# Optimization experiments

Measured on AMD Instinct MI355X. Metric: run time of the kernel, lower is better.

## Reference

```python
import jax, jax.numpy as jnp
import numpy as np

SR_CUT = 10.0
N_ATOMS = 10000
N_PAIRS = 250000
K = 128          # radial basis size
H = 128          # interaction / output hidden width
NB = 5           # num_blocks
NIL = 2          # num_interaction_layers
NOL = 2          # num_output_layers
NO = 2           # num_outputs


def setup_inputs() -> dict:
    key = jax.random.key(0)
    ks = jax.random.split(key, 10)
    Z = jax.random.randint(ks[0], (N_ATOMS,), 0, 95)
    R = jax.random.normal(ks[1], (N_ATOMS, 3), dtype=jnp.float32) * 3.0
    idx_i = jnp.sort(jax.random.randint(ks[2], (N_PAIRS,), 0, N_ATOMS))
    idx_j = jax.random.randint(ks[3], (N_PAIRS,), 0, N_ATOMS)
    s = 0.05
    iW = jax.random.normal(ks[4], (NB, NIL, H, H), dtype=jnp.float32) * s
    iB = jnp.zeros((NB, NIL, H), dtype=jnp.float32)
    oW = jax.random.normal(ks[5], (NB, NOL, H, H), dtype=jnp.float32) * s
    oB = jnp.zeros((NB, NOL, H), dtype=jnp.float32)
    oWf = jax.random.normal(ks[6], (NB, H, NO), dtype=jnp.float32) * s
    oBf = jnp.zeros((NB, NO), dtype=jnp.float32)
    scales = jnp.ones((NO, 95), dtype=jnp.float32)
    shifts = jnp.zeros((NO, 95), dtype=jnp.float32)
    return {"Z": Z, "R": R, "idx_i": idx_i, "idx_j": idx_j,
            "iW": iW, "iB": iB, "oW": oW, "oB": oB,
            "oWf": oWf, "oBf": oBf, "scales": scales, "shifts": shifts}


def _ssp(x):
    # shifted softplus: softplus(x) - log(2)
    return jax.nn.softplus(x) - jnp.log(2.0).astype(x.dtype)


def _basis(rij):
    # smooth polynomial cutoff + Gaussian basis on exp(-r) (PhysNet-style 'Default' radial basis)
    x = rij / SR_CUT
    fcut = jnp.where(rij < SR_CUT, 1.0 - 6.0 * x**5 + 15.0 * x**4 - 10.0 * x**3, 0.0)
    mu = jnp.linspace(np.exp(-SR_CUT), 1.0, K, dtype=rij.dtype)          # [K]
    width = ((2.0 / K) * (1.0 - np.exp(-SR_CUT))) ** (-2)
    er = jnp.exp(-rij)[:, None]                                          # [P,1]
    return fcut[:, None] * jnp.exp(-width * (er - mu) ** 2)              # [P,K]


def reference(Z, R, idx_i, idx_j, iW, iB, oW, oB, oWf, oBf, scales, shifts):
    # pairwise distances via gather (bf_layer.getPairs)
    D = R[idx_j] - R[idx_i]                                              # [P,3]
    rij = jnp.sqrt(jnp.sum(D * D, axis=-1) + 1e-12)                      # [P]
    bf = _basis(rij)                                                     # [P,K]

    x = bf
    outputs = jnp.zeros((N_ATOMS, NO), dtype=R.dtype)
    nhloss = jnp.zeros((), dtype=R.dtype)
    lastout2 = None
    for b in range(NB):
        # interaction block: per-edge MLP (K==H so stacked weights are uniform)
        for l in range(NIL):
            x = _ssp(x @ iW[b, l] + iB[b, l])
        # output block: per-edge MLP + final linear head
        y = x
        for l in range(NOL):
            y = _ssp(y @ oW[b, l] + oB[b, l])
        out_e = y @ oWf[b] + oBf[b]                                      # [P,NO]
        out = jax.ops.segment_sum(out_e, idx_i, num_segments=N_ATOMS)    # [N,NO]
        outputs = outputs + out
        out2 = out ** 2
        if b > 0:
            nhloss = nhloss + jnp.mean(out2 / (out2 + lastout2 + 1e-7))
        lastout2 = out2

    sc = scales[:, Z].T                                                  # [N,NO]
    sh = shifts[:, Z].T                                                  # [N,NO]
    outputs = outputs * sc + sh
    return outputs, rij, nhloss
```

## Files before the change

kernel.cpp:

```cpp
#include <hip/hip_runtime.h>
#include <stdint.h>

#define NP   250000
#define NA   10000
#define NBLK 5
#define NL   20
#define BLOB_W_BYTES 16384
#define BLOB_BYTES   16896

#define LOG2E 1.4426950408889634f
#define LN2   0.6931471805599453f

typedef float  f32x4  __attribute__((ext_vector_type(4)));
typedef unsigned short ushort_t;
typedef unsigned int   uint_t;
typedef int4  i4_ma __attribute__((may_alias));
typedef uint2 u2_ma __attribute__((may_alias));
typedef uint_t u1_ma __attribute__((may_alias));

#if __has_builtin(__builtin_amdgcn_exp2f)
#define FEXP2(x) __builtin_amdgcn_exp2f(x)
#else
#define FEXP2(x) exp2f(x)
#endif
#if __has_builtin(__builtin_amdgcn_logf)
#define FLOG2(x) __builtin_amdgcn_logf(x)
#else
#define FLOG2(x) log2f(x)
#endif

__device__ uint8_t g_blob[NL * BLOB_BYTES];
__device__ float   g_outs[NBLK * NA * 2];
__device__ float   g_nh[1];
__device__ float   g_Rf[NA * 3];
__device__ float   g_oWfF[NBLK * 128 * 2];
__device__ float   g_oBfF[NBLK * 2];
__device__ float   g_scF[190];
__device__ float   g_shF[190];

static __device__ __forceinline__ float bf2f(ushort_t u) {
    return __uint_as_float(((uint_t)u) << 16);
}
static __device__ uint8_t f2fp8(float f) {
    uint_t u = __float_as_uint(f);
    uint8_t s = (uint8_t)((u >> 24) & 0x80);
    float af = fabsf(f);
    if (af != af) return (uint8_t)(s | 0x7F);
    if (af > 448.0f) return (uint8_t)(s | 0x7E);
    int e = (int)((u >> 23) & 0xFF) - 127;
    uint_t m = u & 0x7FFFFFu;
    if (e >= -6) {
        uint_t mant = m >> 20;
        uint_t rest = m & 0xFFFFFu;
        if (rest > 0x80000u || (rest == 0x80000u && (mant & 1u))) mant++;
        uint_t ee = (uint_t)(e + 7);
        if (mant == 8u) { mant = 0u; ee++; }
        if (ee > 15u || (ee == 15u && mant > 6u)) return (uint8_t)(s | 0x7E);
        return (uint8_t)(s | (ee << 3) | mant);
    }
    int qq = (int)rintf(af * 512.0f);
    if (qq > 7) return (uint8_t)(s | 0x08);
    return (uint8_t)(s | (uint_t)qq);
}
template <bool HI>
static __device__ __forceinline__ int cvtpk2(float a, float b, int old) {
#if __has_builtin(__builtin_amdgcn_cvt_pk_fp8_f32)
    return __builtin_amdgcn_cvt_pk_fp8_f32(a, b, old, HI);
#else
    int p = (int)f2fp8(a) | ((int)f2fp8(b) << 8);
    return HI ? (int)((old & 0x0000FFFF) | ((uint_t)p << 16))
              : (int)((old & 0xFFFF0000) | (uint_t)p);
#endif
}
static __device__ __forceinline__ long u2l(u2_ma v) {
    union { u2_ma u; long l; } x; x.u = v; return x.l;
}
static __device__ __forceinline__ float ssp_u(float accv) {
    return FLOG2(0.5f + FEXP2(accv));
}

static __device__ __forceinline__ bool detect_is_f32(const ushort_t* probe) {
    __shared__ int flag;
    if (threadIdx.x == 0) flag = 0;
    __syncthreads();
    if (threadIdx.x < 256) {
        float v = fabsf(bf2f(probe[2 * threadIdx.x]));
        if (!(v <= 64.0f)) flag = 1;
    }
    __syncthreads();
    return flag != 0;
}
static __device__ __forceinline__ float in_elt(const void* p, int i, bool isf32) {
    return isf32 ? ((const float*)p)[i] : bf2f(((const ushort_t*)p)[i]);
}

__global__ void prep_weights(const void* __restrict__ iW, const void* __restrict__ iB,
                             const void* __restrict__ oW, const void* __restrict__ oB)
{
    const bool isf32 = detect_is_f32((const ushort_t*)iW);
    const int L = blockIdx.x >> 2;
    const int qr = blockIdx.x & 3;
    const int b = L >> 2, li = L & 3;
    const void* srcW = (li < 2) ? iW : oW;
    const void* srcB = (li < 2) ? iB : oB;
    const int lyr = (li < 2) ? (b * 2 + li) : (b * 2 + li - 2);
    const int wofs = lyr * 16384;
    const int bofs = lyr * 128;
    uint8_t* blob = g_blob + (size_t)L * BLOB_BYTES;
    uint8_t* dw = blob;
    float*   db = (float*)(blob + BLOB_W_BYTES);
    for (int t = threadIdx.x; t < 4096; t += blockDim.x) {
        int idx = qr * 4096 + t;
        int k = idx >> 7, n = idx & 127;
        float w = in_elt(srcW, wofs + k * 128 + n, isf32);
        if (L == 0) w *= LOG2E;
        dw[n * 128 + 8 * ((k >> 3) ^ (n & 15)) + (k & 7)] = f2fp8(w);
    }
    if (qr == 0)
        for (int m = threadIdx.x; m < 128; m += blockDim.x)
            db[m] = in_elt(srcB, bofs + m, isf32) * LOG2E - 1.0f;
}

__global__ void prep_misc(const void* __restrict__ R, const void* __restrict__ oWf,
                          const void* __restrict__ oBf, const void* __restrict__ scales,
                          const void* __restrict__ shifts, const void* __restrict__ iW)
{
    const bool isf32 = detect_is_f32((const ushort_t*)iW);
    const int t = blockIdx.x * 256 + threadIdx.x;
    if (t < NBLK * NA * 2) g_outs[t] = 0.0f;
    if (t == 0)          g_nh[0]  = 0.0f;
    if (t < NA * 3)      g_Rf[t]   = in_elt(R, t, isf32);
    if (t < NBLK * 256)  g_oWfF[t] = LN2 * in_elt(oWf, t, isf32);
    if (t < NBLK * 2)    g_oBfF[t] = in_elt(oBf, t, isf32);
    if (t < 190)         g_scF[t]  = in_elt(scales, t, isf32);
    if (t < 190)         g_shF[t]  = in_elt(shifts, t, isf32);
}

__global__ __launch_bounds__(256, 3)
void pairs_mlp_kernel(const int* __restrict__ idx_i,
                      const int* __restrict__ idx_j,
                      float* __restrict__ out_rij)
{
    __shared__ i4_ma w_lds[1024];
    __shared__ u2_ma act_all[4 * 512];

    const int wave = threadIdx.x >> 6;
    const int lane = threadIdx.x & 63;
    u2_ma* act = act_all + wave * 512;
    const u2_ma* wl2 = (const u2_ma*)w_lds;

    const int pp = lane & 31;
    const int p0 = blockIdx.x * 128 + wave * 32;
    const int p = p0 + pp;
    const bool valid = (p < NP);

    int ai = 0, aj = 0;
    if (valid) { ai = idx_i[p]; aj = idx_j[p]; }
    float xi0 = g_Rf[3 * ai + 0], xi1 = g_Rf[3 * ai + 1], xi2 = g_Rf[3 * ai + 2];
    float xj0 = g_Rf[3 * aj + 0], xj1 = g_Rf[3 * aj + 1], xj2 = g_Rf[3 * aj + 2];
    float dx = xj0 - xi0, dy = xj1 - xi1, dz = xj2 - xi2;
    float rij = sqrtf(dx * dx + dy * dy + dz * dz + 1e-12f);
    if (lane < 32 && valid) out_rij[p] = rij;

    float fcut = 0.0f;
    if (valid && rij < 10.0f) {
        float xc = rij * 0.1f;
        float x3 = xc * xc * xc;
        fcut = 1.0f + x3 * (-10.0f + xc * (15.0f - 6.0f * xc));
    }
    const float mu0 = 4.5399929762484854e-05f;
    const float dmu = (1.0f - mu0) / 127.0f;
    const float wc = (2.0f / 128.0f) * (1.0f - mu0);
    const float NW2 = -(1.0f / (wc * wc)) * LOG2E;
    float er = FEXP2(-rij * LOG2E);

    const int q = lane >> 4;
    const int l15 = lane & 15;
    const int aseg = valid ? ai : -1;

    u2_ma bfrX[2][4];
    {
        float er_n[2], fc_n[2];
        er_n[0] = __shfl(er, l15, 64);      fc_n[0] = __shfl(fcut, l15, 64);
        er_n[1] = __shfl(er, 16 + l15, 64); fc_n[1] = __shfl(fcut, 16 + l15, 64);
#pragma unroll
        for (int nt = 0; nt < 2; ++nt)
#pragma unroll
            for (int kt = 0; kt < 4; ++kt) {
                float v[8];
#pragma unroll
                for (int jj = 0; jj < 8; ++jj) {
                    int g = kt * 32 + q * 8 + jj;
                    float mu = mu0 + (float)g * dmu;
                    float e0 = er_n[nt] - mu;
                    v[jj] = fc_n[nt] * FEXP2(NW2 * e0 * e0);
                }
                int w0 = cvtpk2<false>(v[0], v[1], 0);
                w0 = cvtpk2<true>(v[2], v[3], w0);
                int w1 = cvtpk2<false>(v[4], v[5], 0);
                w1 = cvtpk2<true>(v[6], v[7], w1);
                bfrX[nt][kt].x = (uint_t)w0;
                bfrX[nt][kt].y = (uint_t)w1;
            }
    }

    for (int blk = 0; blk < NBLK; ++blk) {
#pragma unroll
        for (int li = 0; li < 4; ++li) {
            const int L = blk * 4 + li;
            const i4_ma* gW = (const i4_ma*)(g_blob + (size_t)L * BLOB_BYTES);
            const float* bb = (const float*)(g_blob + (size_t)L * BLOB_BYTES + BLOB_W_BYTES);

            __syncthreads();
#pragma unroll
            for (int it = 0; it < 4; ++it)
                w_lds[threadIdx.x + it * 256] = gW[threadIdx.x + it * 256];
            __syncthreads();

            f32x4 acc[2][8];
#pragma unroll
            for (int mt = 0; mt < 8; ++mt) {
                const f32x4 bias = *(const f32x4*)(bb + mt * 16 + q * 4);
                acc[0][mt] = bias;
                acc[1][mt] = bias;
            }
#pragma unroll
            for (int kt = 0; kt < 4; ++kt) {
                const int cc = kt * 4 + q;
                u2_ma b0, b1;
                if (li == 0) {
                    b0 = bfrX[0][kt];
                    b1 = bfrX[1][kt];
                } else {
                    b0 = act[(l15) * 16 + (cc ^ l15)];
                    b1 = act[(16 + l15) * 16 + (cc ^ l15)];
                    if (li == 2) { bfrX[0][kt] = b0; bfrX[1][kt] = b1; }
                }
                const long lb0 = u2l(b0), lb1 = u2l(b1);
#pragma unroll
                for (int mt = 0; mt < 8; ++mt) {
                    const long la = u2l(wl2[(mt * 16 + l15) * 16 + (cc ^ l15)]);
                    acc[0][mt] = __builtin_amdgcn_mfma_f32_16x16x32_fp8_fp8(
                        la, lb0, acc[0][mt], 0, 0, 0);
                    acc[1][mt] = __builtin_amdgcn_mfma_f32_16x16x32_fp8_fp8(
                        la, lb1, acc[1][mt], 0, 0, 0);
                }
            }

            if (li < 3) {
#pragma unroll
                for (int mt = 0; mt < 8; ++mt) {
                    const int c = mt * 2 + (q >> 1);
#pragma unroll
                    for (int nt = 0; nt < 2; ++nt) {
                        float u0 = ssp_u(acc[nt][mt][0]);
                        float u1 = ssp_u(acc[nt][mt][1]);
                        float u2 = ssp_u(acc[nt][mt][2]);
                        float u3 = ssp_u(acc[nt][mt][3]);
                        int w = cvtpk2<false>(u0, u1, 0);
                        w = cvtpk2<true>(u2, u3, w);
                        const int rp = nt * 16 + l15;
                        ((u1_ma*)&act[rp * 16 + (c ^ (rp & 15))])[q & 1] = (uint_t)w;
                    }
                }
            } else {
                const float* hw = g_oWfF + blk * 256;
                const float ob0 = g_oBfF[blk * 2 + 0];
                const float ob1 = g_oBfF[blk * 2 + 1];
                float hs[2][2];
#pragma unroll
                for (int nt = 0; nt < 2; ++nt) {
                    float h0 = 0.f, h1 = 0.f;
#pragma unroll
                    for (int mt = 0; mt < 8; ++mt) {
#pragma unroll
                        for (int rr = 0; rr < 4; ++rr) {
                            float u = ssp_u(acc[nt][mt][rr]);
                            const int f = mt * 16 + q * 4 + rr;
                            h0 = fmaf(u, hw[f * 2 + 0], h0);
                            h1 = fmaf(u, hw[f * 2 + 1], h1);
                        }
                    }
                    h0 += __shfl_xor(h0, 16, 64);
                    h0 += __shfl_xor(h0, 32, 64);
                    h1 += __shfl_xor(h1, 16, 64);
                    h1 += __shfl_xor(h1, 32, 64);
                    hs[nt][0] = h0; hs[nt][1] = h1;
                }
                float c0v = (pp < 16) ? hs[0][0] : hs[1][0];
                float c1v = (pp < 16) ? hs[0][1] : hs[1][1];
                c0v += ob0; c1v += ob1;
#pragma unroll
                for (int d = 1; d < 32; d <<= 1) {
                    float t0 = __shfl_up(c0v, d, 64);
                    float t1 = __shfl_up(c1v, d, 64);
                    int   an = __shfl_up(aseg, d, 64);
                    if (pp >= d && an == aseg) { c0v += t0; c1v += t1; }
                }
                int ain = __shfl_down(aseg, 1, 64);
                bool tail = (pp == 31) || (ain != aseg);
                if (lane < 32 && valid && tail) {
                    atomicAdd(&g_outs[(blk * NA + aseg) * 2 + 0], c0v);
                    atomicAdd(&g_outs[(blk * NA + aseg) * 2 + 1], c1v);
                }
            }
        }
    }
}

__global__ void finalize_kernel(const int* __restrict__ Z,
                                float* __restrict__ out_atoms)
{
    __shared__ float red[256];
    const int a = blockIdx.x * 256 + threadIdx.x;
    float s = 0.f;
    if (a < NA) {
        float v[NBLK][2];
        float t0 = 0.f, t1 = 0.f;
#pragma unroll
        for (int b = 0; b < NBLK; ++b) {
            v[b][0] = g_outs[(b * NA + a) * 2 + 0];
            v[b][1] = g_outs[(b * NA + a) * 2 + 1];
            t0 += v[b][0]; t1 += v[b][1];
        }
        const int z = Z[a];
        out_atoms[a * 2 + 0] = t0 * g_scF[z]      + g_shF[z];
        out_atoms[a * 2 + 1] = t1 * g_scF[95 + z] + g_shF[95 + z];
#pragma unroll
        for (int b = 1; b < NBLK; ++b)
#pragma unroll
            for (int o = 0; o < 2; ++o) {
                float x2 = v[b][o] * v[b][o];
                float p2 = v[b - 1][o] * v[b - 1][o];
                s += x2 / (x2 + p2 + 1e-7f);
            }
    }
    red[threadIdx.x] = s;
    __syncthreads();
    for (int st = 128; st > 0; st >>= 1) {
        if (threadIdx.x < st) red[threadIdx.x] += red[threadIdx.x + st];
        __syncthreads();
    }
    if (threadIdx.x == 0) atomicAdd(&g_nh[0], red[0]);
}

__global__ void nh_write(float* __restrict__ out_nh)
{
    out_nh[0] = g_nh[0] * (1.0f / 20000.0f);
}

extern "C" void kernel_launch(void* const* d_in, const int* in_sizes, int n_in,
                              void* d_out, int out_size, void* d_ws, size_t ws_size,
                              hipStream_t stream)
{
    const int* Z     = (const int*)d_in[0];
    const void* R    = d_in[1];
    const int* idx_i = (const int*)d_in[2];
    const int* idx_j = (const int*)d_in[3];
    const void* iW   = d_in[4];
    const void* iB   = d_in[5];
    const void* oW   = d_in[6];
    const void* oB   = d_in[7];
    const void* oWf  = d_in[8];
    const void* oBf  = d_in[9];
    const void* scales = d_in[10];
    const void* shifts = d_in[11];

    float* out_f = (float*)d_out;

    prep_weights<<<NL * 4, 256, 0, stream>>>(iW, iB, oW, oB);
    prep_misc<<<(NBLK * NA * 2 + 255) / 256, 256, 0, stream>>>(R, oWf, oBf, scales, shifts, iW);
    pairs_mlp_kernel<<<(NP + 127) / 128, 256, 0, stream>>>(idx_i, idx_j, out_f + 2 * NA);
    finalize_kernel<<<(NA + 255) / 256, 256, 0, stream>>>(Z, out_f);
    nh_write<<<1, 1, 0, stream>>>(out_f + 2 * NA + NP);
}
```

Before: 279.6 us.

## Halve per-wave pair tile to 16 pairs and raise occupancy to four blocks

Each wave now handles 16 pairs instead of 32. Accumulators, activation LDS and basis registers are halved, and launch bounds are raised to allow 4 blocks per CU. The weight prep kernel now packs four fp8 weights per 32-bit store instead of writing single bytes, and the bias is fed directly as the first MFMA accumulator. The trade-off is that each weight tile staged in LDS is reused across half as many pairs, so weight loads and barriers per pair double, in exchange for lower register pressure and more waves resident.

```diff
diff --git a/kernel.cpp b/kernel.cpp
--- a/kernel.cpp
+++ b/kernel.cpp
@@ -107,14 +107,19 @@
     const int wofs = lyr * 16384;
     const int bofs = lyr * 128;
     uint8_t* blob = g_blob + (size_t)L * BLOB_BYTES;
-    uint8_t* dw = blob;
-    float*   db = (float*)(blob + BLOB_W_BYTES);
-    for (int t = threadIdx.x; t < 4096; t += blockDim.x) {
-        int idx = qr * 4096 + t;
-        int k = idx >> 7, n = idx & 127;
-        float w = in_elt(srcW, wofs + k * 128 + n, isf32);
-        if (L == 0) w *= LOG2E;
-        dw[n * 128 + 8 * ((k >> 3) ^ (n & 15)) + (k & 7)] = f2fp8(w);
+    uint_t* dw = (uint_t*)blob;
+    float*  db = (float*)(blob + BLOB_W_BYTES);
+    const float sc = (L == 0) ? LOG2E : 1.0f;
+    for (int t = threadIdx.x; t < 1024; t += blockDim.x) {
+        int d = qr * 1024 + t;
+        int n = d & 127, kg = d >> 7;
+        float w0 = sc * in_elt(srcW, wofs + (kg * 4 + 0) * 128 + n, isf32);
+        float w1 = sc * in_elt(srcW, wofs + (kg * 4 + 1) * 128 + n, isf32);
+        float w2 = sc * in_elt(srcW, wofs + (kg * 4 + 2) * 128 + n, isf32);
+        float w3 = sc * in_elt(srcW, wofs + (kg * 4 + 3) * 128 + n, isf32);
+        int w = cvtpk2<false>(w0, w1, 0);
+        w = cvtpk2<true>(w2, w3, w);
+        dw[n * 32 + 2 * ((kg >> 1) ^ (n & 15)) + (kg & 1)] = (uint_t)w;
     }
     if (qr == 0)
         for (int m = threadIdx.x; m < 128; m += blockDim.x)
@@ -136,22 +141,23 @@
     if (t < 190)         g_shF[t]  = in_elt(shifts, t, isf32);
 }
 
-__global__ __launch_bounds__(256, 3)
+__global__ __launch_bounds__(256, 4)
 void pairs_mlp_kernel(const int* __restrict__ idx_i,
                       const int* __restrict__ idx_j,
                       float* __restrict__ out_rij)
 {
     __shared__ i4_ma w_lds[1024];
-    __shared__ u2_ma act_all[4 * 512];
+    __shared__ u2_ma act_all[4 * 256];
 
     const int wave = threadIdx.x >> 6;
     const int lane = threadIdx.x & 63;
-    u2_ma* act = act_all + wave * 512;
+    u2_ma* act = act_all + wave * 256;
     const u2_ma* wl2 = (const u2_ma*)w_lds;
 
-    const int pp = lane & 31;
-    const int p0 = blockIdx.x * 128 + wave * 32;
-    const int p = p0 + pp;
+    const int q = lane >> 4;
+    const int l15 = lane & 15;
+    const int p0 = blockIdx.x * 64 + wave * 16;
+    const int p = p0 + l15;
     const bool valid = (p < NP);
 
     int ai = 0, aj = 0;
@@ -160,7 +166,7 @@
     float xj0 = g_Rf[3 * aj + 0], xj1 = g_Rf[3 * aj + 1], xj2 = g_Rf[3 * aj + 2];
     float dx = xj0 - xi0, dy = xj1 - xi1, dz = xj2 - xi2;
     float rij = sqrtf(dx * dx + dy * dy + dz * dz + 1e-12f);
-    if (lane < 32 && valid) out_rij[p] = rij;
+    if (lane < 16 && valid) out_rij[p] = rij;
 
     float fcut = 0.0f;
     if (valid && rij < 10.0f) {
@@ -174,34 +180,25 @@
     const float NW2 = -(1.0f / (wc * wc)) * LOG2E;
     float er = FEXP2(-rij * LOG2E);
 
-    const int q = lane >> 4;
-    const int l15 = lane & 15;
     const int aseg = valid ? ai : -1;
 
-    u2_ma bfrX[2][4];
-    {
-        float er_n[2], fc_n[2];
-        er_n[0] = __shfl(er, l15, 64);      fc_n[0] = __shfl(fcut, l15, 64);
-        er_n[1] = __shfl(er, 16 + l15, 64); fc_n[1] = __shfl(fcut, 16 + l15, 64);
-#pragma unroll
-        for (int nt = 0; nt < 2; ++nt)
-#pragma unroll
-            for (int kt = 0; kt < 4; ++kt) {
-                float v[8];
-#pragma unroll
-                for (int jj = 0; jj < 8; ++jj) {
-                    int g = kt * 32 + q * 8 + jj;
-                    float mu = mu0 + (float)g * dmu;
-                    float e0 = er_n[nt] - mu;
-                    v[jj] = fc_n[nt] * FEXP2(NW2 * e0 * e0);
-                }
-                int w0 = cvtpk2<false>(v[0], v[1], 0);
-                w0 = cvtpk2<true>(v[2], v[3], w0);
-                int w1 = cvtpk2<false>(v[4], v[5], 0);
-                w1 = cvtpk2<true>(v[6], v[7], w1);
-                bfrX[nt][kt].x = (uint_t)w0;
-                bfrX[nt][kt].y = (uint_t)w1;
-            }
+    u2_ma bfrX[4];
+#pragma unroll
+    for (int kt = 0; kt < 4; ++kt) {
+        float v[8];
+#pragma unroll
+        for (int jj = 0; jj < 8; ++jj) {
+            int g = kt * 32 + q * 8 + jj;
+            float mu = mu0 + (float)g * dmu;
+            float e0 = er - mu;
+            v[jj] = fcut * FEXP2(NW2 * e0 * e0);
+        }
+        int w0 = cvtpk2<false>(v[0], v[1], 0);
+        w0 = cvtpk2<true>(v[2], v[3], w0);
+        int w1 = cvtpk2<false>(v[4], v[5], 0);
+        w1 = cvtpk2<true>(v[6], v[7], w1);
+        bfrX[kt].x = (uint_t)w0;
+        bfrX[kt].y = (uint_t)w1;
     }
 
     for (int blk = 0; blk < NBLK; ++blk) {
@@ -217,33 +214,28 @@
                 w_lds[threadIdx.x + it * 256] = gW[threadIdx.x + it * 256];
             __syncthreads();
 
-            f32x4 acc[2][8];
-#pragma unroll
-            for (int mt = 0; mt < 8; ++mt) {
-                const f32x4 bias = *(const f32x4*)(bb + mt * 16 + q * 4);
-                acc[0][mt] = bias;
-                acc[1][mt] = bias;
-            }
+            f32x4 bias[8];
+#pragma unroll
+            for (int mt = 0; mt < 8; ++mt)
+                bias[mt] = *(const f32x4*)(bb + mt * 16 + q * 4);
+
+            f32x4 acc[8];
 #pragma unroll
             for (int kt = 0; kt < 4; ++kt) {
                 const int cc = kt * 4 + q;
-                u2_ma b0, b1;
+                u2_ma b0;
                 if (li == 0) {
-                    b0 = bfrX[0][kt];
-                    b1 = bfrX[1][kt];
+                    b0 = bfrX[kt];
                 } else {
-                    b0 = act[(l15) * 16 + (cc ^ l15)];
-                    b1 = act[(16 + l15) * 16 + (cc ^ l15)];
-                    if (li == 2) { bfrX[0][kt] = b0; bfrX[1][kt] = b1; }
-                }
-                const long lb0 = u2l(b0), lb1 = u2l(b1);
+                    b0 = act[l15 * 16 + (cc ^ l15)];
+                    if (li == 2) bfrX[kt] = b0;
+                }
+                const long lb0 = u2l(b0);
 #pragma unroll
                 for (int mt = 0; mt < 8; ++mt) {
                     const long la = u2l(wl2[(mt * 16 + l15) * 16 + (cc ^ l15)]);
-                    acc[0][mt] = __builtin_amdgcn_mfma_f32_16x16x32_fp8_fp8(
-                        la, lb0, acc[0][mt], 0, 0, 0);
-                    acc[1][mt] = __builtin_amdgcn_mfma_f32_16x16x32_fp8_fp8(
-                        la, lb1, acc[1][mt], 0, 0, 0);
+                    acc[mt] = __builtin_amdgcn_mfma_f32_16x16x32_fp8_fp8(
+                        la, lb0, (kt == 0) ? bias[mt] : acc[mt], 0, 0, 0);
                 }
             }
 
@@ -251,55 +243,45 @@
 #pragma unroll
                 for (int mt = 0; mt < 8; ++mt) {
                     const int c = mt * 2 + (q >> 1);
-#pragma unroll
-                    for (int nt = 0; nt < 2; ++nt) {
-                        float u0 = ssp_u(acc[nt][mt][0]);
-                        float u1 = ssp_u(acc[nt][mt][1]);
-                        float u2 = ssp_u(acc[nt][mt][2]);
-                        float u3 = ssp_u(acc[nt][mt][3]);
-                        int w = cvtpk2<false>(u0, u1, 0);
-                        w = cvtpk2<true>(u2, u3, w);
-                        const int rp = nt * 16 + l15;
-                        ((u1_ma*)&act[rp * 16 + (c ^ (rp & 15))])[q & 1] = (uint_t)w;
-                    }
+                    float u0 = ssp_u(acc[mt][0]);
+                    float u1 = ssp_u(acc[mt][1]);
+                    float u2 = ssp_u(acc[mt][2]);
+                    float u3 = ssp_u(acc[mt][3]);
+                    int w = cvtpk2<false>(u0, u1, 0);
+                    w = cvtpk2<true>(u2, u3, w);
+                    ((u1_ma*)&act[l15 * 16 + (c ^ l15)])[q & 1] = (uint_t)w;
                 }
             } else {
                 const float* hw = g_oWfF + blk * 256;
                 const float ob0 = g_oBfF[blk * 2 + 0];
                 const float ob1 = g_oBfF[blk * 2 + 1];
-                float hs[2][2];
-#pragma unroll
-                for (int nt = 0; nt < 2; ++nt) {
-                    float h0 = 0.f, h1 = 0.f;
-#pragma unroll
-                    for (int mt = 0; mt < 8; ++mt) {
-#pragma unroll
-                        for (int rr = 0; rr < 4; ++rr) {
-                            float u = ssp_u(acc[nt][mt][rr]);
-                            const int f = mt * 16 + q * 4 + rr;
-                            h0 = fmaf(u, hw[f * 2 + 0], h0);
-                            h1 = fmaf(u, hw[f * 2 + 1], h1);
-                        }
+                float h0 = 0.f, h1 = 0.f;
+#pragma unroll
+                for (int mt = 0; mt < 8; ++mt) {
+#pragma unroll
+                    for (int rr = 0; rr < 4; ++rr) {
+                        float u = ssp_u(acc[mt][rr]);
+                        const int f = mt * 16 + q * 4 + rr;
+                        h0 = fmaf(u, hw[f * 2 + 0], h0);
+                        h1 = fmaf(u, hw[f * 2 + 1], h1);
                     }
-                    h0 += __shfl_xor(h0, 16, 64);
-                    h0 += __shfl_xor(h0, 32, 64);
-                    h1 += __shfl_xor(h1, 16, 64);
-                    h1 += __shfl_xor(h1, 32, 64);
-                    hs[nt][0] = h0; hs[nt][1] = h1;
-                }
-                float c0v = (pp < 16) ? hs[0][0] : hs[1][0];
-                float c1v = (pp < 16) ? hs[0][1] : hs[1][1];
-                c0v += ob0; c1v += ob1;
-#pragma unroll
-                for (int d = 1; d < 32; d <<= 1) {
+                }
+                h0 += __shfl_xor(h0, 16, 64);
+                h0 += __shfl_xor(h0, 32, 64);
+                h1 += __shfl_xor(h1, 16, 64);
+                h1 += __shfl_xor(h1, 32, 64);
+                float c0v = h0 + ob0;
+                float c1v = h1 + ob1;
+#pragma unroll
+                for (int d = 1; d < 16; d <<= 1) {
                     float t0 = __shfl_up(c0v, d, 64);
                     float t1 = __shfl_up(c1v, d, 64);
                     int   an = __shfl_up(aseg, d, 64);
-                    if (pp >= d && an == aseg) { c0v += t0; c1v += t1; }
+                    if (lane >= d && an == aseg) { c0v += t0; c1v += t1; }
                 }
                 int ain = __shfl_down(aseg, 1, 64);
-                bool tail = (pp == 31) || (ain != aseg);
-                if (lane < 32 && valid && tail) {
+                bool tail = (lane == 15) || (ain != aseg);
+                if (lane < 16 && valid && tail) {
                     atomicAdd(&g_outs[(blk * NA + aseg) * 2 + 0], c0v);
                     atomicAdd(&g_outs[(blk * NA + aseg) * 2 + 1], c1v);
                 }
@@ -370,7 +352,7 @@
 
     prep_weights<<<NL * 4, 256, 0, stream>>>(iW, iB, oW, oB);
     prep_misc<<<(NBLK * NA * 2 + 255) / 256, 256, 0, stream>>>(R, oWf, oBf, scales, shifts, iW);
-    pairs_mlp_kernel<<<(NP + 127) / 128, 256, 0, stream>>>(idx_i, idx_j, out_f + 2 * NA);
+    pairs_mlp_kernel<<<(NP + 63) / 64, 256, 0, stream>>>(idx_i, idx_j, out_f + 2 * NA);
     finalize_kernel<<<(NA + 255) / 256, 256, 0, stream>>>(Z, out_f);
     nh_write<<<1, 1, 0, stream>>>(out_f + 2 * NA + NP);
 }
```

Result: slower. 312.7 us (+11.8%).

## Read fp8 weight fragments directly from global memory instead of staging through LDS

Applied to the files above, without the earlier changes.

Removes the per-layer cooperative copy of the 16KB fp8 weight tile into shared memory and the two block-wide barriers around it. Each wave now loads its MFMA A-operand fragments straight from the global blob, relying on L1/L2 caching since all blocks read the same weights. The bias is fed as the initial accumulator only on the first k-step, saving register copies. The weight prep kernel is also changed to pack four fp8 values per 32-bit store. This trades LDS traffic and synchronisation for global/L2 load latency on the critical MFMA path, and it frees shared memory.

```diff
diff --git a/kernel.cpp b/kernel.cpp
--- a/kernel.cpp
+++ b/kernel.cpp
@@ -107,14 +107,19 @@
     const int wofs = lyr * 16384;
     const int bofs = lyr * 128;
     uint8_t* blob = g_blob + (size_t)L * BLOB_BYTES;
-    uint8_t* dw = blob;
-    float*   db = (float*)(blob + BLOB_W_BYTES);
-    for (int t = threadIdx.x; t < 4096; t += blockDim.x) {
-        int idx = qr * 4096 + t;
-        int k = idx >> 7, n = idx & 127;
-        float w = in_elt(srcW, wofs + k * 128 + n, isf32);
-        if (L == 0) w *= LOG2E;
-        dw[n * 128 + 8 * ((k >> 3) ^ (n & 15)) + (k & 7)] = f2fp8(w);
+    uint_t* dw = (uint_t*)blob;
+    float*  db = (float*)(blob + BLOB_W_BYTES);
+    const float sc = (L == 0) ? LOG2E : 1.0f;
+    for (int t = threadIdx.x; t < 1024; t += blockDim.x) {
+        int d = qr * 1024 + t;
+        int n = d & 127, kg = d >> 7;
+        float w0 = sc * in_elt(srcW, wofs + (kg * 4 + 0) * 128 + n, isf32);
+        float w1 = sc * in_elt(srcW, wofs + (kg * 4 + 1) * 128 + n, isf32);
+        float w2 = sc * in_elt(srcW, wofs + (kg * 4 + 2) * 128 + n, isf32);
+        float w3 = sc * in_elt(srcW, wofs + (kg * 4 + 3) * 128 + n, isf32);
+        int w = cvtpk2<false>(w0, w1, 0);
+        w = cvtpk2<true>(w2, w3, w);
+        dw[n * 32 + 2 * ((kg >> 1) ^ (n & 15)) + (kg & 1)] = (uint_t)w;
     }
     if (qr == 0)
         for (int m = threadIdx.x; m < 128; m += blockDim.x)
@@ -141,13 +146,11 @@
                       const int* __restrict__ idx_j,
                       float* __restrict__ out_rij)
 {
-    __shared__ i4_ma w_lds[1024];
     __shared__ u2_ma act_all[4 * 512];
 
     const int wave = threadIdx.x >> 6;
     const int lane = threadIdx.x & 63;
     u2_ma* act = act_all + wave * 512;
-    const u2_ma* wl2 = (const u2_ma*)w_lds;
 
     const int pp = lane & 31;
     const int p0 = blockIdx.x * 128 + wave * 32;
@@ -208,22 +211,15 @@
 #pragma unroll
         for (int li = 0; li < 4; ++li) {
             const int L = blk * 4 + li;
-            const i4_ma* gW = (const i4_ma*)(g_blob + (size_t)L * BLOB_BYTES);
+            const u2_ma* wg2 = (const u2_ma*)(g_blob + (size_t)L * BLOB_BYTES);
             const float* bb = (const float*)(g_blob + (size_t)L * BLOB_BYTES + BLOB_W_BYTES);
 
-            __syncthreads();
-#pragma unroll
-            for (int it = 0; it < 4; ++it)
-                w_lds[threadIdx.x + it * 256] = gW[threadIdx.x + it * 256];
-            __syncthreads();
+            f32x4 bias[8];
+#pragma unroll
+            for (int mt = 0; mt < 8; ++mt)
+                bias[mt] = *(const f32x4*)(bb + mt * 16 + q * 4);
 
             f32x4 acc[2][8];
-#pragma unroll
-            for (int mt = 0; mt < 8; ++mt) {
-                const f32x4 bias = *(const f32x4*)(bb + mt * 16 + q * 4);
-                acc[0][mt] = bias;
-                acc[1][mt] = bias;
-            }
 #pragma unroll
             for (int kt = 0; kt < 4; ++kt) {
                 const int cc = kt * 4 + q;
@@ -239,11 +235,11 @@
                 const long lb0 = u2l(b0), lb1 = u2l(b1);
 #pragma unroll
                 for (int mt = 0; mt < 8; ++mt) {
-                    const long la = u2l(wl2[(mt * 16 + l15) * 16 + (cc ^ l15)]);
+                    const long la = u2l(wg2[(mt * 16 + l15) * 16 + (cc ^ l15)]);
                     acc[0][mt] = __builtin_amdgcn_mfma_f32_16x16x32_fp8_fp8(
-                        la, lb0, acc[0][mt], 0, 0, 0);
+                        la, lb0, (kt == 0) ? bias[mt] : acc[0][mt], 0, 0, 0);
                     acc[1][mt] = __builtin_amdgcn_mfma_f32_16x16x32_fp8_fp8(
-                        la, lb1, acc[1][mt], 0, 0, 0);
+                        la, lb1, (kt == 0) ? bias[mt] : acc[1][mt], 0, 0, 0);
                 }
             }
 
```

Result: slower. 427.4 us (+52.8%).
